# Kernel optimization log

Measured on AMD Instinct MI355X. Metric: run time of the kernel, lower is better.

## Reference

```python
import jax, jax.numpy as jnp
import numpy as np

SYLL_V, WORD_V, K = 10000, 20000, 10
SYLL_D, WORD_D, H = 64, 32, 64  # H = hidden_dim // 2 per direction
B, T = 256, 512
IN_D = SYLL_D + WORD_D


def lstm_dir(x, w_ih, w_hh, b_ih, b_hh, reverse):
    # x: [B,T,D]; w_ih: [4H,D]; w_hh: [4H,H]; PyTorch gate order i,f,g,o
    b, t, _ = x.shape
    h = w_hh.shape[1]
    xp = jnp.einsum('btd,gd->btg', x, w_ih) + b_ih + b_hh  # [B,T,4H]
    if reverse:
        xp = xp[:, ::-1]
    def step(carry, xt):
        hs, cs = carry
        g = xt + hs @ w_hh.T
        i, f, gg, o = jnp.split(g, 4, axis=-1)
        i = jax.nn.sigmoid(i); f = jax.nn.sigmoid(f)
        gg = jnp.tanh(gg); o = jax.nn.sigmoid(o)
        cs = f * cs + i * gg
        hs = o * jnp.tanh(cs)
        return (hs, cs), hs
    h0 = jnp.zeros((b, h), x.dtype)
    _, hseq = jax.lax.scan(step, (h0, h0), jnp.swapaxes(xp, 0, 1))
    hseq = jnp.swapaxes(hseq, 0, 1)  # [B,T,H]
    if reverse:
        hseq = hseq[:, ::-1]
    return hseq


def crf_llh(emissions, tags, mask, start_t, end_t, trans):
    # torchcrf log-likelihood, batch_first. emissions [B,T,K], tags [B,T], mask [B,T] bool
    b, t, k = emissions.shape
    mf = mask.astype(emissions.dtype)
    ar = jnp.arange(b)
    # numerator: score of the given tag path
    num = start_t[tags[:, 0]] + emissions[ar, 0, tags[:, 0]]
    e_tag = jnp.take_along_axis(emissions, tags[:, :, None], axis=2)[:, :, 0]  # [B,T]
    tr = trans[tags[:, :-1], tags[:, 1:]]  # [B,T-1]
    num = num + jnp.sum(mf[:, 1:] * (tr + e_tag[:, 1:]), axis=1)
    seq_len = jnp.sum(mask.astype(jnp.int32), axis=1)
    last_tags = jnp.take_along_axis(tags, (seq_len - 1)[:, None], axis=1)[:, 0]
    num = num + end_t[last_tags]
    # denominator: log partition via forward algorithm (sequential logsumexp scan)
    alpha0 = start_t[None, :] + emissions[:, 0]  # [B,K]
    def step(alpha, inp):
        em_t, m_t = inp  # [B,K], [B]
        nxt = jax.nn.logsumexp(alpha[:, :, None] + trans[None] + em_t[:, None, :], axis=1)
        return jnp.where(m_t[:, None], nxt, alpha), None
    alpha, _ = jax.lax.scan(
        step, alpha0,
        (jnp.swapaxes(emissions[:, 1:], 0, 1), jnp.swapaxes(mask[:, 1:], 0, 1)))
    den = jax.nn.logsumexp(alpha + end_t[None, :], axis=1)
    return num - den


def setup_inputs() -> dict:
    key = jax.random.key(0)
    ks = jax.random.split(key, 20)
    s = 0.1
    syll_emb = jax.random.normal(ks[0], (SYLL_V, SYLL_D), jnp.float32) * s
    syll_emb = syll_emb.at[0].set(0.0)  # padding_idx
    word_emb = jax.random.normal(ks[1], (WORD_V, WORD_D), jnp.float32) * s
    word_emb = word_emb.at[0].set(0.0)
    def lstm_params(i):
        return (jax.random.normal(ks[i], (4 * H, IN_D), jnp.float32) * s,
                jax.random.normal(ks[i + 1], (4 * H, H), jnp.float32) * s,
                jax.random.normal(ks[i + 2], (4 * H,), jnp.float32) * s,
                jax.random.normal(ks[i + 3], (4 * H,), jnp.float32) * s)
    w_ih_f, w_hh_f, b_ih_f, b_hh_f = lstm_params(2)
    w_ih_b, w_hh_b, b_ih_b, b_hh_b = lstm_params(6)
    W_tag = jax.random.normal(ks[10], (K, 2 * H), jnp.float32) * s
    b_tag = jax.random.normal(ks[11], (K,), jnp.float32) * s
    crf_start = jax.random.normal(ks[12], (K,), jnp.float32) * s
    crf_end = jax.random.normal(ks[13], (K,), jnp.float32) * s
    crf_trans = jax.random.normal(ks[14], (K, K), jnp.float32) * s
    return {
        'syll_input': jax.random.randint(ks[15], (B, T), 0, SYLL_V),
        'word_input': jax.random.randint(ks[16], (B, T), 0, WORD_V),
        'tags': jax.random.randint(ks[17], (B, T), 0, K),
        'mask': jnp.ones((B, T), jnp.bool_),
        'syll_emb': syll_emb, 'word_emb': word_emb,
        'w_ih_f': w_ih_f, 'w_hh_f': w_hh_f, 'b_ih_f': b_ih_f, 'b_hh_f': b_hh_f,
        'w_ih_b': w_ih_b, 'w_hh_b': w_hh_b, 'b_ih_b': b_ih_b, 'b_hh_b': b_hh_b,
        'W_tag': W_tag, 'b_tag': b_tag,
        'crf_start': crf_start, 'crf_end': crf_end, 'crf_trans': crf_trans,
    }


def reference(syll_input, word_input, tags, mask,
              syll_emb, word_emb,
              w_ih_f, w_hh_f, b_ih_f, b_hh_f,
              w_ih_b, w_hh_b, b_ih_b, b_hh_b,
              W_tag, b_tag, crf_start, crf_end, crf_trans):
    combined = jnp.concatenate([syll_emb[syll_input], word_emb[word_input]], axis=2)  # [B,T,96]
    h_f = lstm_dir(combined, w_ih_f, w_hh_f, b_ih_f, b_hh_f, reverse=False)
    h_b = lstm_dir(combined, w_ih_b, w_hh_b, b_ih_b, b_hh_b, reverse=True)
    lstm_out = jnp.concatenate([h_f, h_b], axis=2)  # [B,T,128]
    emissions = jnp.einsum('bth,kh->btk', lstm_out, W_tag) + b_tag
    llh = crf_llh(emissions, tags, mask, crf_start, crf_end, crf_trans)
    return -jnp.mean(llh)  # reduction='mean', negated
```

## Files before the change

kernel.cpp:

```cpp
#include <hip/hip_runtime.h>

typedef unsigned short ushort_t;
typedef unsigned int uint_t;
typedef __attribute__((ext_vector_type(8))) short short8;
typedef __attribute__((ext_vector_type(4))) float f32x4;
typedef __fp16 fp16x2 __attribute__((ext_vector_type(2)));
typedef __fp16 fp16x4 __attribute__((ext_vector_type(4)));

#define B_SZ 256
#define T_LEN 512
#define Hd 64
#define IND 96
#define G4 256
#define KT 10
#define SYLL_V 10000
#define WORD_V 20000
#define TP 520

#define L2E  1.4426950408889634f
#define L2E2 2.8853900817779268f

#define U16_PS_F 0
#define U16_PS_B (SYLL_V*G4)
#define U16_PW_F (2*SYLL_V*G4)
#define U16_PW_B (2*SYLL_V*G4 + WORD_V*G4)
#define U16_TAB_END (2*SYLL_V*G4 + 2*WORD_V*G4)
#define F_EM   (U16_TAB_END/2)
#define F_OMEGA (F_EM + B_SZ*T_LEN*KT)
#define F_S1   (F_OMEGA + B_SZ*64*100)
#define F_END  (F_S1 + B_SZ*64)
#define F_OFFS (F_END + (B_SZ*T_LEN*2*Hd)/2)
#define F_WBUF (F_OFFS + 2*B_SZ*TP*2)
#define F_BIAS (F_WBUF + 49152*4)

template <int V> struct ic { static constexpr int v = V; };

__device__ __forceinline__ ushort_t f2bf(float f) {
    uint_t u = __float_as_uint(f);
    uint_t r = (u + 0x7FFFu + ((u >> 16) & 1u)) >> 16;
    return (ushort_t)r;
}
__device__ __forceinline__ short8 cvt8(const float* p) {
    float4 x0 = *(const float4*)&p[0];
    float4 x1 = *(const float4*)&p[4];
    short8 f;
    f[0] = (short)f2bf(x0.x); f[1] = (short)f2bf(x0.y);
    f[2] = (short)f2bf(x0.z); f[3] = (short)f2bf(x0.w);
    f[4] = (short)f2bf(x1.x); f[5] = (short)f2bf(x1.y);
    f[6] = (short)f2bf(x1.z); f[7] = (short)f2bf(x1.w);
    return f;
}
__device__ __forceinline__ short8 cvt8s(const float* p, float sc) {
    float4 x0 = *(const float4*)&p[0];
    float4 x1 = *(const float4*)&p[4];
    short8 f;
    f[0] = (short)f2bf(x0.x*sc); f[1] = (short)f2bf(x0.y*sc);
    f[2] = (short)f2bf(x0.z*sc); f[3] = (short)f2bf(x0.w*sc);
    f[4] = (short)f2bf(x1.x*sc); f[5] = (short)f2bf(x1.y*sc);
    f[6] = (short)f2bf(x1.z*sc); f[7] = (short)f2bf(x1.w*sc);
    return f;
}

__global__ __launch_bounds__(256) void wprep_kernel(
    const float* __restrict__ w_ih_f, const float* __restrict__ w_ih_b,
    const float* __restrict__ b_ih_f, const float* __restrict__ b_hh_f,
    const float* __restrict__ b_ih_b, const float* __restrict__ b_hh_b,
    short8* __restrict__ wbuf, float* __restrict__ biasbuf)
{
    const int dir = blockIdx.x;
    const float* __restrict__ wih = dir ? w_ih_b : w_ih_f;
    const float* __restrict__ bi = dir ? b_ih_b : b_ih_f;
    const float* __restrict__ bh = dir ? b_hh_b : b_hh_f;
    const int tid = threadIdx.x;
    const int w = tid >> 6;
    const int l = tid & 63;
    const int rg = l >> 4;
    const int c = l & 15;

    {
        int s = tid;
        int g = 64 * (s & 3) + (s >> 2);
        float gsc = ((s & 3) == 2) ? L2E2 : -L2E;
        biasbuf[dir * 256 + s] = 0.5f * (bi[g] + bh[g]) * gsc;
    }
#pragma unroll
    for (int mt = 0; mt < 4; mt++) {
        int s = 64 * w + 16 * mt + c;
        int g = 64 * (s & 3) + (s >> 2);
        float gsc = ((s & 3) == 2) ? L2E2 : -L2E;
#pragma unroll
        for (int ch = 0; ch < 3; ch++) {
            const float* wp = &wih[g * 96 + ch * 32 + rg * 8];
            float4 x0 = *(const float4*)&wp[0];
            float4 x1 = *(const float4*)&wp[4];
            float vv[8] = {x0.x, x0.y, x0.z, x0.w, x1.x, x1.y, x1.z, x1.w};
            short8 h8, l8;
#pragma unroll
            for (int j = 0; j < 8; j++) {
                float sv = vv[j] * gsc;
                ushort_t hb2 = f2bf(sv);
                h8[j] = (short)hb2;
                l8[j] = (short)f2bf(sv - __uint_as_float((uint_t)hb2 << 16));
            }
            int base = (((dir * 4 + w) * 4 + mt) * 3 + ch) * 2;
            wbuf[(size_t)(base + 0) * 64 + l] = h8;
            wbuf[(size_t)(base + 1) * 64 + l] = l8;
        }
    }
}

__global__ __launch_bounds__(128) void offs_kernel(
    const int* __restrict__ syll, const int* __restrict__ word,
    int2* __restrict__ offs)
{
    const int bid = blockIdx.x;
    const int dir = bid & 1;
    const int b = bid >> 1;
    int2* __restrict__ o = offs + (size_t)(dir * B_SZ + b) * TP;
    for (int t = threadIdx.x; t < TP; t += 128) {
        int tc = t > T_LEN - 1 ? T_LEN - 1 : t;
        int p = dir ? (T_LEN - 1 - tc) : tc;
        int2 v;
        v.x = syll[b * T_LEN + p] << 9;
        v.y = word[b * T_LEN + p] << 9;
        o[t] = v;
    }
}

template <int D, int CH0, int NCH>
__global__ __launch_bounds__(256) void proj_mfma(
    const float* __restrict__ emb,
    const short8* __restrict__ wbuf, const float* __restrict__ biasbuf,
    ushort_t* __restrict__ out_f, ushort_t* __restrict__ out_b)
{
    const int dir = blockIdx.y;
    ushort_t* __restrict__ out = dir ? out_b : out_f;
    const int v0 = blockIdx.x * 16;
    const int tid = threadIdx.x;
    const int w = tid >> 6;
    const int l = tid & 63;
    const int rg = l >> 4;
    const int c = l & 15;

    __shared__ __align__(16) ushort_t Xh[16][D + 8];
    for (int i = tid; i < 16 * D; i += 256) {
        int row = i / D, k = i - row * D;
        Xh[row][k] = f2bf(emb[(size_t)v0 * D + i]);
    }

    short8 Ah[4][NCH], Al[4][NCH];
    f32x4 bias[4];
#pragma unroll
    for (int mt = 0; mt < 4; mt++) {
#pragma unroll
        for (int ch = 0; ch < NCH; ch++) {
            int base = (((dir * 4 + w) * 4 + mt) * 3 + (CH0 + ch)) * 2;
            Ah[mt][ch] = wbuf[(size_t)(base + 0) * 64 + l];
            Al[mt][ch] = wbuf[(size_t)(base + 1) * 64 + l];
        }
        bias[mt] = *(const f32x4*)&biasbuf[dir * 256 + 64 * w + 16 * mt + 4 * rg];
    }
    __syncthreads();

#pragma unroll
    for (int mt = 0; mt < 4; mt++) {
        f32x4 acc = bias[mt];
#pragma unroll
        for (int ch = 0; ch < NCH; ch++) {
            short8 Bf = *(const short8*)&Xh[c][ch * 32 + rg * 8];
            acc = __builtin_amdgcn_mfma_f32_16x16x32_bf16(Ah[mt][ch], Bf, acc, 0, 0, 0);
            acc = __builtin_amdgcn_mfma_f32_16x16x32_bf16(Al[mt][ch], Bf, acc, 0, 0, 0);
        }
        fp16x2 p0 = __builtin_amdgcn_cvt_pkrtz(acc[0], acc[1]);
        fp16x2 p1 = __builtin_amdgcn_cvt_pkrtz(acc[2], acc[3]);
        uint2 o;
        o.x = *(uint_t*)&p0;
        o.y = *(uint_t*)&p1;
        *(uint2*)&out[(size_t)(v0 + c) * G4 + 64 * w + 16 * mt + 4 * rg] = o;
    }
}

__global__ __launch_bounds__(256, 1) void lstm_kernel(
    const float* __restrict__ w_hh_f, const float* __restrict__ w_hh_b,
    const ushort_t* __restrict__ tab_u16, const int2* __restrict__ offs,
    ushort_t* __restrict__ h_out)
{
    const int dir = blockIdx.x & 1;
    const int bA = (blockIdx.x >> 1) * 4;
    const int tid = threadIdx.x;
    const int w = tid >> 6;
    const int l = tid & 63;
    const int rg = l >> 4;
    const int c = l & 15;
    const int cell = 16 * w + c;
    const int celloff = cell * 8;

    const char* __restrict__ tsb = (const char*)(tab_u16 + (dir ? U16_PS_B : U16_PS_F));
    const char* __restrict__ twb = (const char*)(tab_u16 + (dir ? U16_PW_B : U16_PW_F));
    const float* __restrict__ whh = dir ? w_hh_b : w_hh_f;

    short8 bfrag[4][2];
#pragma unroll
    for (int tau = 0; tau < 4; tau++) {
        const float sc = (tau == 2) ? L2E2 : -L2E;
#pragma unroll
        for (int chk = 0; chk < 2; chk++)
            bfrag[tau][chk] = cvt8s(whh + (size_t)(64 * tau + cell) * Hd + chk * 32 + rg * 8, sc);
    }

    __shared__ __align__(16) ushort_t h_lds[2][16][72];
    for (int i = tid; i < 2 * 16 * 72; i += 256) ((ushort_t*)h_lds)[i] = 0;

    const int chain = bA + rg;
    const int p0 = dir ? (T_LEN - 1) : 0;
    const int2* __restrict__ op = offs + (size_t)(dir * B_SZ + chain) * TP;

    fp16x4 tS[4], tW[4];
    int2 ix[4];
#pragma unroll
    for (int j = 0; j < 4; j++) {
        int2 o = op[j];
        tS[j] = *(const fp16x4*)(tsb + ((size_t)o.x + celloff));
        tW[j] = *(const fp16x4*)(twb + ((size_t)o.y + celloff));
        ix[j] = op[j + 4];
    }

    float cst = 0.f;
    ushort_t* hp = h_out + ((size_t)(chain * T_LEN + p0) * 2 + dir) * Hd + cell;
    const int hstep = dir ? -128 : 128;
    const f32x4 zro = {0.f, 0.f, 0.f, 0.f};
    __syncthreads();

    auto step = [&](auto STC, int t) {
        constexpr int ST = decltype(STC)::v;
        fp16x4 pp = tS[ST] + tW[ST];
        float ps0 = (float)pp[0];
        float ps1 = (float)pp[1];
        float ps2 = (float)pp[2];
        float ps3 = (float)pp[3];
        tS[ST] = *(const fp16x4*)(tsb + ((size_t)ix[ST].x + celloff));
        tW[ST] = *(const fp16x4*)(twb + ((size_t)ix[ST].y + celloff));
        ix[ST] = op[t + 8];

        f32x4 cc0 = {ps0, 0.f, 0.f, 0.f};
        f32x4 cc1 = {ps1, 0.f, 0.f, 0.f};
        f32x4 cc2 = {ps2, 0.f, 0.f, 0.f};
        f32x4 cc3 = {ps3, 0.f, 0.f, 0.f};
        const ushort_t* hrow = &h_lds[t & 1][c][0];
        short8 a0 = *(const short8*)(hrow + rg * 8);
        short8 a1 = *(const short8*)(hrow + 32 + rg * 8);
        f32x4 p00 = __builtin_amdgcn_mfma_f32_16x16x32_bf16(a0, bfrag[0][0], cc0, 0, 0, 0);
        f32x4 p10 = __builtin_amdgcn_mfma_f32_16x16x32_bf16(a0, bfrag[1][0], cc1, 0, 0, 0);
        f32x4 p20 = __builtin_amdgcn_mfma_f32_16x16x32_bf16(a0, bfrag[2][0], cc2, 0, 0, 0);
        f32x4 p30 = __builtin_amdgcn_mfma_f32_16x16x32_bf16(a0, bfrag[3][0], cc3, 0, 0, 0);
        f32x4 p01 = __builtin_amdgcn_mfma_f32_16x16x32_bf16(a1, bfrag[0][1], zro, 0, 0, 0);
        f32x4 p11 = __builtin_amdgcn_mfma_f32_16x16x32_bf16(a1, bfrag[1][1], zro, 0, 0, 0);
        f32x4 p21 = __builtin_amdgcn_mfma_f32_16x16x32_bf16(a1, bfrag[2][1], zro, 0, 0, 0);
        f32x4 p31 = __builtin_amdgcn_mfma_f32_16x16x32_bf16(a1, bfrag[3][1], zro, 0, 0, 0);

        float ai = p00[0] + p01[0];
        float af = p10[0] + p11[0];
        float ag = fminf(p20[0] + p21[0], 60.0f);
        float ao = p30[0] + p31[0];
        float ei = __builtin_amdgcn_exp2f(ai);
        float ef = __builtin_amdgcn_exp2f(af);
        float Eg = __builtin_amdgcn_exp2f(ag);
        float eo = __builtin_amdgcn_exp2f(ao);
        float e3 = 1.0f + ef;
        float pe = (1.0f + ei) * (1.0f + Eg);
        float num = __builtin_fmaf(Eg - 1.0f, e3, cst * pe);
        float cn = num * __builtin_amdgcn_rcpf(e3 * pe);
        cst = cn;
        float t2 = fminf(cn * L2E2, 60.0f);
        float E2 = __builtin_amdgcn_exp2f(t2);
        float h = (E2 - 1.0f) * __builtin_amdgcn_rcpf((1.0f + eo) * (1.0f + E2));

        ushort_t hb = f2bf(h);
        h_lds[(t + 1) & 1][4 * rg][cell] = hb;
        *hp = hb;
        hp += hstep;
        __builtin_amdgcn_sched_barrier(0);
        asm volatile("s_waitcnt lgkmcnt(0)" ::: "memory");
        __builtin_amdgcn_s_barrier();
        __builtin_amdgcn_sched_barrier(0);
    };

    for (int t = 0; t < T_LEN; t += 4) {
        step(ic<0>{}, t);
        step(ic<1>{}, t + 1);
        step(ic<2>{}, t + 2);
        step(ic<3>{}, t + 3);
    }
}

#define EMIS_G 4
__global__ __launch_bounds__(64) void emis_kernel(
    const ushort_t* __restrict__ hseq, const float* __restrict__ W_tag,
    const float* __restrict__ b_tag, float* __restrict__ em)
{
    const int l = threadIdx.x;
    const int rg = l >> 4;
    const int n = l & 15;

    short8 bf[4];
#pragma unroll
    for (int ch = 0; ch < 4; ch++) {
        if (n < KT) bf[ch] = cvt8(W_tag + (size_t)n * 128 + ch * 32 + rg * 8);
        else { short8 z = {0,0,0,0,0,0,0,0}; bf[ch] = z; }
    }
    const float btv = (n < KT) ? b_tag[n] : 0.f;

#pragma unroll
    for (int gi = 0; gi < EMIS_G; gi++) {
        const int row0 = (blockIdx.x * EMIS_G + gi) * 16;
        const ushort_t* __restrict__ ar = hseq + (size_t)(row0 + n) * 128 + rg * 8;
        short8 a0 = *(const short8*)&ar[0];
        short8 a1 = *(const short8*)&ar[32];
        short8 a2 = *(const short8*)&ar[64];
        short8 a3 = *(const short8*)&ar[96];
        f32x4 acc = {btv, btv, btv, btv};
        acc = __builtin_amdgcn_mfma_f32_16x16x32_bf16(a0, bf[0], acc, 0, 0, 0);
        acc = __builtin_amdgcn_mfma_f32_16x16x32_bf16(a1, bf[1], acc, 0, 0, 0);
        acc = __builtin_amdgcn_mfma_f32_16x16x32_bf16(a2, bf[2], acc, 0, 0, 0);
        acc = __builtin_amdgcn_mfma_f32_16x16x32_bf16(a3, bf[3], acc, 0, 0, 0);
        if (n < KT) {
#pragma unroll
            for (int r = 0; r < 4; r++)
                em[(size_t)(row0 + 4 * rg + r) * KT + n] = acc[r];
        }
    }
}

__global__ __launch_bounds__(64) void crf_stage1(
    const float* __restrict__ em, const float* __restrict__ trans,
    float* __restrict__ Omega, float* __restrict__ S1)
{
    __shared__ float etT[KT * 12];
    const int tid = threadIdx.x;
    for (int i = tid; i < KT * 12; i += 64) etT[i] = 0.f;
    __syncthreads();
    for (int i = tid; i < 100; i += 64) {
        int jj = i / 10, k = i % 10;
        etT[k * 12 + jj] = __expf(trans[i]);
    }
    __syncthreads();

    const int id = blockIdx.x * 64 + tid;
    const int b = id >> 6, c = id & 63;
    const int t0 = (c == 0) ? 1 : c * 8;
    const int nt = (c == 0) ? 7 : 8;

    float run[10][10];
    float s = 0.f;

    float ecur[10];
    {
        const float* r = em + (size_t)(b * T_LEN + t0) * KT;
#pragma unroll
        for (int k = 0; k < 10; k++) ecur[k] = r[k];
    }
    {
        float mx = ecur[0];
#pragma unroll
        for (int k = 1; k < 10; k++) mx = fmaxf(mx, ecur[k]);
        s += mx;
        float ee[10];
#pragma unroll
        for (int k = 0; k < 10; k++) ee[k] = __expf(ecur[k] - mx);
#pragma unroll
        for (int jj = 0; jj < 10; jj++)
#pragma unroll
            for (int k = 0; k < 10; k++) run[jj][k] = etT[k * 12 + jj] * ee[k];
    }
    float enx[10];
    if (nt > 1) {
        const float* r = em + (size_t)(b * T_LEN + t0 + 1) * KT;
#pragma unroll
        for (int k = 0; k < 10; k++) enx[k] = r[k];
    }
    for (int li = 1; li < nt; li++) {
        float mx = enx[0];
#pragma unroll
        for (int k = 1; k < 10; k++) mx = fmaxf(mx, enx[k]);
        s += mx;
        float ee[10];
#pragma unroll
        for (int k = 0; k < 10; k++) ee[k] = __expf(enx[k] - mx);
        if (li + 1 < nt) {
            const float* r = em + (size_t)(b * T_LEN + t0 + li + 1) * KT;
#pragma unroll
            for (int k = 0; k < 10; k++) enx[k] = r[k];
        }
#pragma unroll
        for (int i = 0; i < 10; i++) {
            float outp[10];
#pragma unroll
            for (int k = 0; k < 10; k++) {
                float sum = 0.f;
#pragma unroll
                for (int jj = 0; jj < 10; jj++) sum += run[i][jj] * etT[k * 12 + jj];
                outp[k] = sum * ee[k];
            }
#pragma unroll
            for (int k = 0; k < 10; k++) run[i][k] = outp[k];
        }
    }
    float m = run[0][0];
#pragma unroll
    for (int i = 0; i < 10; i++)
#pragma unroll
        for (int k = 0; k < 10; k++) m = fmaxf(m, run[i][k]);
    float inv = 1.0f / m;
    s += __logf(m);
#pragma unroll
    for (int i = 0; i < 10; i++)
#pragma unroll
        for (int k = 0; k < 10; k++) Omega[(size_t)id * 100 + i * 10 + k] = run[i][k] * inv;
    S1[id] = s;
}

__global__ __launch_bounds__(256) void crf_stage2(
    const float* __restrict__ Omega, const float* __restrict__ S1,
    const float* __restrict__ em, const int* __restrict__ tags,
    const float* __restrict__ start_t, const float* __restrict__ end_t,
    const float* __restrict__ trans, float* __restrict__ out)
{
    const int b = blockIdx.x;
    const int tid = threadIdx.x;
    __shared__ float bufA[64 * 120];
    __shared__ float bufB[32 * 120];
    __shared__ float sh_red[4];
    __shared__ float sh_s;
    __shared__ float scl_sh[32];
    __shared__ float lg_sh[32];
    __shared__ float lg_acc_sh;

    for (int idx = tid; idx < 6400; idx += 256) {
        int c = idx / 100, e = idx % 100;
        bufA[c * 120 + (e / 10) * 12 + (e % 10)] = Omega[(size_t)(b * 64 + c) * 100 + e];
    }
    if (tid < 64) {
        float v = S1[b * 64 + tid];
        for (int off = 32; off; off >>= 1) v += __shfl_down(v, off);
        if (tid == 0) sh_s = v;
    }
    if (tid == 0) lg_acc_sh = 0.f;
    __syncthreads();

    float* src = bufA;
    float* dst = bufB;
    for (int n = 32; n >= 1; n >>= 1) {
        for (int idx = tid; idx < n * 100; idx += 256) {
            int p = idx / 100, e = idx % 100, i = e / 10, k = e % 10;
            const float* A = src + (2 * p) * 120;
            const float* Bm = src + (2 * p + 1) * 120;
            float sum = 0.f;
#pragma unroll
            for (int jj = 0; jj < 10; jj++) sum += A[i * 12 + jj] * Bm[jj * 12 + k];
            dst[p * 120 + i * 12 + k] = sum;
        }
        __syncthreads();
        if (n == 32 || n == 8 || n == 2) {
            if (tid < n) {
                const float* M = dst + tid * 120;
                float mx = 0.f;
                for (int i = 0; i < 10; i++)
                    for (int k = 0; k < 10; k++) mx = fmaxf(mx, M[i * 12 + k]);
                scl_sh[tid] = 1.0f / mx;
                lg_sh[tid] = __logf(mx);
            }
            __syncthreads();
            if (tid == 0) {
                float s = 0.f;
                for (int p = 0; p < n; p++) s += lg_sh[p];
                lg_acc_sh += s;
            }
            for (int idx = tid; idx < n * 100; idx += 256) {
                int p = idx / 100, e = idx % 100;
                dst[p * 120 + (e / 10) * 12 + (e % 10)] *= scl_sh[p];
            }
            __syncthreads();
        }
        float* t_ = src; src = dst; dst = t_;
    }

    float den = 0.f;
    if (tid < 64) {
        float val = 0.f;
        float mx0 = 0.f;
        if (tid < 10) {
            mx0 = -1e30f;
            for (int jj = 0; jj < 10; jj++) mx0 = fmaxf(mx0, start_t[jj] + em[(size_t)(b * T_LEN) * KT + jj]);
            for (int jj = 0; jj < 10; jj++) {
                float v0 = __expf(start_t[jj] + em[(size_t)(b * T_LEN) * KT + jj] - mx0);
                val += v0 * src[jj * 12 + tid];
            }
            val *= __expf(end_t[tid]);
        }
        for (int off = 8; off; off >>= 1) val += __shfl_down(val, off);
        if (tid == 0) den = __logf(val) + mx0 + sh_s + lg_acc_sh;
    }

    float part = 0.f;
    const int* __restrict__ tg = tags + b * T_LEN;
    for (int t = tid; t < T_LEN; t += 256) {
        int cur = tg[t];
        if (t == 0) part += start_t[cur] + em[(size_t)(b * T_LEN) * KT + cur];
        else part += trans[tg[t - 1] * KT + cur] + em[(size_t)(b * T_LEN + t) * KT + cur];
        if (t == T_LEN - 1) part += end_t[cur];
    }
    for (int off = 32; off; off >>= 1) part += __shfl_down(part, off);
    if ((tid & 63) == 0) sh_red[tid >> 6] = part;
    __syncthreads();
    if (tid == 0) {
        float num = sh_red[0] + sh_red[1] + sh_red[2] + sh_red[3];
        float llh = num - den;
        atomicAdd(out, llh * (-1.0f / 256.0f));
    }
}

extern "C" void kernel_launch(void* const* d_in, const int* in_sizes, int n_in,
                              void* d_out, int out_size, void* d_ws, size_t ws_size,
                              hipStream_t stream) {
    const int* syll      = (const int*)d_in[0];
    const int* word      = (const int*)d_in[1];
    const int* tags      = (const int*)d_in[2];
    const float* syll_emb = (const float*)d_in[4];
    const float* word_emb = (const float*)d_in[5];
    const float* w_ih_f  = (const float*)d_in[6];
    const float* w_hh_f  = (const float*)d_in[7];
    const float* b_ih_f  = (const float*)d_in[8];
    const float* b_hh_f  = (const float*)d_in[9];
    const float* w_ih_b  = (const float*)d_in[10];
    const float* w_hh_b  = (const float*)d_in[11];
    const float* b_ih_b  = (const float*)d_in[12];
    const float* b_hh_b  = (const float*)d_in[13];
    const float* W_tag   = (const float*)d_in[14];
    const float* b_tag   = (const float*)d_in[15];
    const float* crf_start = (const float*)d_in[16];
    const float* crf_end   = (const float*)d_in[17];
    const float* crf_trans = (const float*)d_in[18];

    float* out = (float*)d_out;
    float* ws = (float*)d_ws;
    ushort_t* tab = (ushort_t*)ws;
    ushort_t* hseq = (ushort_t*)(ws + F_END);
    int2* offs = (int2*)(ws + F_OFFS);
    short8* wbuf = (short8*)(ws + F_WBUF);
    float* biasbuf = ws + F_BIAS;

    hipMemsetAsync(d_out, 0, sizeof(float), stream);

    wprep_kernel<<<2, 256, 0, stream>>>(
        w_ih_f, w_ih_b, b_ih_f, b_hh_f, b_ih_b, b_hh_b, wbuf, biasbuf);

    offs_kernel<<<B_SZ * 2, 128, 0, stream>>>(syll, word, offs);

    proj_mfma<64, 0, 2><<<dim3(SYLL_V / 16, 2), 256, 0, stream>>>(
        syll_emb, wbuf, biasbuf, tab + U16_PS_F, tab + U16_PS_B);
    proj_mfma<32, 2, 1><<<dim3(WORD_V / 16, 2), 256, 0, stream>>>(
        word_emb, wbuf, biasbuf, tab + U16_PW_F, tab + U16_PW_B);

    lstm_kernel<<<B_SZ * 2 / 4, 256, 0, stream>>>(
        w_hh_f, w_hh_b, tab, offs, hseq);

    emis_kernel<<<B_SZ * T_LEN / (16 * EMIS_G), 64, 0, stream>>>(
        hseq, W_tag, b_tag, ws + F_EM);

    crf_stage1<<<256, 64, 0, stream>>>(ws + F_EM, crf_trans, ws + F_OMEGA, ws + F_S1);

    crf_stage2<<<B_SZ, 256, 0, stream>>>(
        ws + F_OMEGA, ws + F_S1, ws + F_EM, tags, crf_start, crf_end, crf_trans, out);
}
```

Baseline: 304.0 us.

## Fuse emission projection and both CRF stages into one kernel using LDS

Replaces the emission kernel and the two CRF stage kernels with a single kernel in which each block handles two batch rows. Emissions are computed with MFMA into shared memory, the chunked transfer-matrix products run in registers, and the tree reduction reuses the same LDS buffer. This removes two kernel launches and the global round trips for emissions, Omega and S1. In exchange the grid drops to 128 blocks of 256 threads with large LDS use, so fewer waves are in flight, and only half the threads do the stage-1 work.

Measured after the change: 312.3 us. 1.03x slower.

```diff
diff --git a/kernel.cpp b/kernel.cpp
--- a/kernel.cpp
+++ b/kernel.cpp
@@ -25,10 +25,7 @@
 #define U16_PW_F (2*SYLL_V*G4)
 #define U16_PW_B (2*SYLL_V*G4 + WORD_V*G4)
 #define U16_TAB_END (2*SYLL_V*G4 + 2*WORD_V*G4)
-#define F_EM   (U16_TAB_END/2)
-#define F_OMEGA (F_EM + B_SZ*T_LEN*KT)
-#define F_S1   (F_OMEGA + B_SZ*64*100)
-#define F_END  (F_S1 + B_SZ*64)
+#define F_END  (U16_TAB_END/2)
 #define F_OFFS (F_END + (B_SZ*T_LEN*2*Hd)/2)
 #define F_WBUF (F_OFFS + 2*B_SZ*TP*2)
 #define F_BIAS (F_WBUF + 49152*4)
@@ -293,14 +290,34 @@
     }
 }
 
-#define EMIS_G 4
-__global__ __launch_bounds__(64) void emis_kernel(
+__global__ __launch_bounds__(256) void crf_fused(
     const ushort_t* __restrict__ hseq, const float* __restrict__ W_tag,
-    const float* __restrict__ b_tag, float* __restrict__ em)
+    const float* __restrict__ b_tag, const float* __restrict__ trans,
+    const int* __restrict__ tags, const float* __restrict__ start_t,
+    const float* __restrict__ end_t, float* __restrict__ out)
 {
-    const int l = threadIdx.x;
+    const int tid = threadIdx.x;
+    const int w = tid >> 6;
+    const int l = tid & 63;
     const int rg = l >> 4;
     const int n = l & 15;
+
+    __shared__ __align__(16) float em_l[1024 * 12];
+    __shared__ float etT[120];
+    __shared__ float e0_sh[2][10];
+    __shared__ float scl_sh[32];
+    __shared__ float lg_sh[32];
+    __shared__ float sh_s[2];
+    __shared__ float num_sh[2][2];
+    __shared__ float lg_acc;
+    __shared__ float den_sh[2];
+
+    for (int i = tid; i < 120; i += 256) etT[i] = 0.f;
+    __syncthreads();
+    for (int i = tid; i < 100; i += 256) {
+        int jj = i / 10, k = i % 10;
+        etT[k * 12 + jj] = __expf(trans[i]);
+    }
 
     short8 bf[4];
 #pragma unroll
@@ -309,11 +326,11 @@
         else { short8 z = {0,0,0,0,0,0,0,0}; bf[ch] = z; }
     }
     const float btv = (n < KT) ? b_tag[n] : 0.f;
-
-#pragma unroll
-    for (int gi = 0; gi < EMIS_G; gi++) {
-        const int row0 = (blockIdx.x * EMIS_G + gi) * 16;
-        const ushort_t* __restrict__ ar = hseq + (size_t)(row0 + n) * 128 + rg * 8;
+    const size_t gbase = (size_t)blockIdx.x * 1024;
+#pragma unroll 4
+    for (int gi = 0; gi < 16; gi++) {
+        const int row0 = w * 256 + gi * 16;
+        const ushort_t* __restrict__ ar = hseq + (gbase + row0 + n) * 128 + rg * 8;
         short8 a0 = *(const short8*)&ar[0];
         short8 a1 = *(const short8*)&ar[32];
         short8 a2 = *(const short8*)&ar[64];
@@ -326,197 +343,171 @@
         if (n < KT) {
 #pragma unroll
             for (int r = 0; r < 4; r++)
-                em[(size_t)(row0 + 4 * rg + r) * KT + n] = acc[r];
-        }
-    }
-}
-
-__global__ __launch_bounds__(64) void crf_stage1(
-    const float* __restrict__ em, const float* __restrict__ trans,
-    float* __restrict__ Omega, float* __restrict__ S1)
-{
-    __shared__ float etT[KT * 12];
-    const int tid = threadIdx.x;
-    for (int i = tid; i < KT * 12; i += 64) etT[i] = 0.f;
+                em_l[(row0 + 4 * rg + r) * 12 + n] = acc[r];
+        }
+    }
     __syncthreads();
-    for (int i = tid; i < 100; i += 64) {
-        int jj = i / 10, k = i % 10;
-        etT[k * 12 + jj] = __expf(trans[i]);
-    }
-    __syncthreads();
-
-    const int id = blockIdx.x * 64 + tid;
-    const int b = id >> 6, c = id & 63;
-    const int t0 = (c == 0) ? 1 : c * 8;
-    const int nt = (c == 0) ? 7 : 8;
-
+
+    const int bl = tid >> 6;
+    const int c = tid & 63;
+    const bool active = tid < 128;
     float run[10][10];
     float s = 0.f;
-
-    float ecur[10];
+    if (active) {
+        const int t0 = (c == 0) ? 1 : c * 8;
+        const int nt = (c == 0) ? 7 : 8;
+        const float* __restrict__ eb = &em_l[(bl * 512) * 12];
+        float ecur[10];
+#pragma unroll
+        for (int k = 0; k < 10; k++) ecur[k] = eb[t0 * 12 + k];
+        {
+            float mx = ecur[0];
+#pragma unroll
+            for (int k = 1; k < 10; k++) mx = fmaxf(mx, ecur[k]);
+            s += mx;
+            float ee[10];
+#pragma unroll
+            for (int k = 0; k < 10; k++) ee[k] = __expf(ecur[k] - mx);
+#pragma unroll
+            for (int jj = 0; jj < 10; jj++)
+#pragma unroll
+                for (int k = 0; k < 10; k++) run[jj][k] = etT[k * 12 + jj] * ee[k];
+        }
+        for (int li = 1; li < nt; li++) {
+            float enx[10];
+#pragma unroll
+            for (int k = 0; k < 10; k++) enx[k] = eb[(t0 + li) * 12 + k];
+            float mx = enx[0];
+#pragma unroll
+            for (int k = 1; k < 10; k++) mx = fmaxf(mx, enx[k]);
+            s += mx;
+            float ee[10];
+#pragma unroll
+            for (int k = 0; k < 10; k++) ee[k] = __expf(enx[k] - mx);
+#pragma unroll
+            for (int i = 0; i < 10; i++) {
+                float outp[10];
+#pragma unroll
+                for (int k = 0; k < 10; k++) {
+                    float sum = 0.f;
+#pragma unroll
+                    for (int jj = 0; jj < 10; jj++) sum += run[i][jj] * etT[k * 12 + jj];
+                    outp[k] = sum * ee[k];
+                }
+#pragma unroll
+                for (int k = 0; k < 10; k++) run[i][k] = outp[k];
+            }
+        }
+        float m = run[0][0];
+#pragma unroll
+        for (int i = 0; i < 10; i++)
+#pragma unroll
+            for (int k = 0; k < 10; k++) m = fmaxf(m, run[i][k]);
+        float inv = 1.0f / m;
+        s += __logf(m);
+#pragma unroll
+        for (int i = 0; i < 10; i++)
+#pragma unroll
+            for (int k = 0; k < 10; k++) run[i][k] *= inv;
+    }
+
     {
-        const float* r = em + (size_t)(b * T_LEN + t0) * KT;
-#pragma unroll
-        for (int k = 0; k < 10; k++) ecur[k] = r[k];
-    }
-    {
-        float mx = ecur[0];
-#pragma unroll
-        for (int k = 1; k < 10; k++) mx = fmaxf(mx, ecur[k]);
-        s += mx;
-        float ee[10];
-#pragma unroll
-        for (int k = 0; k < 10; k++) ee[k] = __expf(ecur[k] - mx);
-#pragma unroll
-        for (int jj = 0; jj < 10; jj++)
-#pragma unroll
-            for (int k = 0; k < 10; k++) run[jj][k] = etT[k * 12 + jj] * ee[k];
-    }
-    float enx[10];
-    if (nt > 1) {
-        const float* r = em + (size_t)(b * T_LEN + t0 + 1) * KT;
-#pragma unroll
-        for (int k = 0; k < 10; k++) enx[k] = r[k];
-    }
-    for (int li = 1; li < nt; li++) {
-        float mx = enx[0];
-#pragma unroll
-        for (int k = 1; k < 10; k++) mx = fmaxf(mx, enx[k]);
-        s += mx;
-        float ee[10];
-#pragma unroll
-        for (int k = 0; k < 10; k++) ee[k] = __expf(enx[k] - mx);
-        if (li + 1 < nt) {
-            const float* r = em + (size_t)(b * T_LEN + t0 + li + 1) * KT;
-#pragma unroll
-            for (int k = 0; k < 10; k++) enx[k] = r[k];
-        }
-#pragma unroll
-        for (int i = 0; i < 10; i++) {
-            float outp[10];
-#pragma unroll
-            for (int k = 0; k < 10; k++) {
+        const int blc = w >> 1;
+        const int b2 = blockIdx.x * 2 + blc;
+        const float* __restrict__ eb = &em_l[(blc * 512) * 12];
+        const int* __restrict__ tg = tags + b2 * T_LEN;
+        float part = 0.f;
+        for (int t = l + (w & 1) * 64; t < T_LEN; t += 128) {
+            int cur = tg[t];
+            float ev = eb[t * 12 + cur];
+            if (t == 0) part += start_t[cur] + ev;
+            else part += trans[tg[t - 1] * KT + cur] + ev;
+            if (t == T_LEN - 1) part += end_t[cur];
+        }
+        for (int off = 32; off; off >>= 1) part += __shfl_down(part, off);
+        if (l == 0) num_sh[blc][w & 1] = part;
+    }
+    if (tid < 20) {
+        int blc = tid / 10, jj = tid % 10;
+        e0_sh[blc][jj] = em_l[(blc * 512) * 12 + jj];
+    }
+    if (active) {
+        float v = s;
+        for (int off = 32; off; off >>= 1) v += __shfl_down(v, off);
+        if (c == 0) sh_s[bl] = v;
+    }
+
+    float* bufA = em_l;
+    float* bufB = em_l + 7680;
+    float llh_acc = 0.f;
+    for (int blc = 0; blc < 2; blc++) {
+        __syncthreads();
+        if (active && bl == blc) {
+#pragma unroll
+            for (int i = 0; i < 10; i++)
+#pragma unroll
+                for (int k = 0; k < 10; k++) bufA[c * 120 + i * 12 + k] = run[i][k];
+        }
+        if (tid == 0) lg_acc = 0.f;
+        __syncthreads();
+
+        float* src = bufA;
+        float* dst = bufB;
+        for (int nn = 32; nn >= 1; nn >>= 1) {
+            for (int idx = tid; idx < nn * 100; idx += 256) {
+                int p = idx / 100, e = idx % 100, i = e / 10, k = e % 10;
+                const float* A = src + (2 * p) * 120;
+                const float* Bm = src + (2 * p + 1) * 120;
                 float sum = 0.f;
 #pragma unroll
-                for (int jj = 0; jj < 10; jj++) sum += run[i][jj] * etT[k * 12 + jj];
-                outp[k] = sum * ee[k];
-            }
-#pragma unroll
-            for (int k = 0; k < 10; k++) run[i][k] = outp[k];
-        }
-    }
-    float m = run[0][0];
-#pragma unroll
-    for (int i = 0; i < 10; i++)
-#pragma unroll
-        for (int k = 0; k < 10; k++) m = fmaxf(m, run[i][k]);
-    float inv = 1.0f / m;
-    s += __logf(m);
-#pragma unroll
-    for (int i = 0; i < 10; i++)
-#pragma unroll
-        for (int k = 0; k < 10; k++) Omega[(size_t)id * 100 + i * 10 + k] = run[i][k] * inv;
-    S1[id] = s;
-}
-
-__global__ __launch_bounds__(256) void crf_stage2(
-    const float* __restrict__ Omega, const float* __restrict__ S1,
-    const float* __restrict__ em, const int* __restrict__ tags,
-    const float* __restrict__ start_t, const float* __restrict__ end_t,
-    const float* __restrict__ trans, float* __restrict__ out)
-{
-    const int b = blockIdx.x;
-    const int tid = threadIdx.x;
-    __shared__ float bufA[64 * 120];
-    __shared__ float bufB[32 * 120];
-    __shared__ float sh_red[4];
-    __shared__ float sh_s;
-    __shared__ float scl_sh[32];
-    __shared__ float lg_sh[32];
-    __shared__ float lg_acc_sh;
-
-    for (int idx = tid; idx < 6400; idx += 256) {
-        int c = idx / 100, e = idx % 100;
-        bufA[c * 120 + (e / 10) * 12 + (e % 10)] = Omega[(size_t)(b * 64 + c) * 100 + e];
-    }
-    if (tid < 64) {
-        float v = S1[b * 64 + tid];
-        for (int off = 32; off; off >>= 1) v += __shfl_down(v, off);
-        if (tid == 0) sh_s = v;
-    }
-    if (tid == 0) lg_acc_sh = 0.f;
-    __syncthreads();
-
-    float* src = bufA;
-    float* dst = bufB;
-    for (int n = 32; n >= 1; n >>= 1) {
-        for (int idx = tid; idx < n * 100; idx += 256) {
-            int p = idx / 100, e = idx % 100, i = e / 10, k = e % 10;
-            const float* A = src + (2 * p) * 120;
-            const float* Bm = src + (2 * p + 1) * 120;
-            float sum = 0.f;
-#pragma unroll
-            for (int jj = 0; jj < 10; jj++) sum += A[i * 12 + jj] * Bm[jj * 12 + k];
-            dst[p * 120 + i * 12 + k] = sum;
-        }
-        __syncthreads();
-        if (n == 32 || n == 8 || n == 2) {
-            if (tid < n) {
-                const float* M = dst + tid * 120;
-                float mx = 0.f;
-                for (int i = 0; i < 10; i++)
-                    for (int k = 0; k < 10; k++) mx = fmaxf(mx, M[i * 12 + k]);
-                scl_sh[tid] = 1.0f / mx;
-                lg_sh[tid] = __logf(mx);
+                for (int jj = 0; jj < 10; jj++) sum += A[i * 12 + jj] * Bm[jj * 12 + k];
+                dst[p * 120 + i * 12 + k] = sum;
             }
             __syncthreads();
-            if (tid == 0) {
-                float s = 0.f;
-                for (int p = 0; p < n; p++) s += lg_sh[p];
-                lg_acc_sh += s;
+            if (nn == 32 || nn == 8 || nn == 2) {
+                if (tid < nn) {
+                    const float* M = dst + tid * 120;
+                    float mx = 0.f;
+                    for (int i = 0; i < 10; i++)
+                        for (int k = 0; k < 10; k++) mx = fmaxf(mx, M[i * 12 + k]);
+                    scl_sh[tid] = 1.0f / mx;
+                    lg_sh[tid] = __logf(mx);
+                }
+                __syncthreads();
+                if (tid == 0) {
+                    float ssum = 0.f;
+                    for (int p = 0; p < nn; p++) ssum += lg_sh[p];
+                    lg_acc += ssum;
+                }
+                for (int idx = tid; idx < nn * 100; idx += 256) {
+                    int p = idx / 100, e = idx % 100;
+                    dst[p * 120 + (e / 10) * 12 + (e % 10)] *= scl_sh[p];
+                }
+                __syncthreads();
             }
-            for (int idx = tid; idx < n * 100; idx += 256) {
-                int p = idx / 100, e = idx % 100;
-                dst[p * 120 + (e / 10) * 12 + (e % 10)] *= scl_sh[p];
+            float* t_ = src; src = dst; dst = t_;
+        }
+
+        if (tid < 64) {
+            float val = 0.f;
+            float mx0 = 0.f;
+            if (tid < 10) {
+                mx0 = -1e30f;
+                for (int jj = 0; jj < 10; jj++) mx0 = fmaxf(mx0, start_t[jj] + e0_sh[blc][jj]);
+                for (int jj = 0; jj < 10; jj++) {
+                    float v0 = __expf(start_t[jj] + e0_sh[blc][jj] - mx0);
+                    val += v0 * src[jj * 12 + tid];
+                }
+                val *= __expf(end_t[tid]);
             }
-            __syncthreads();
-        }
-        float* t_ = src; src = dst; dst = t_;
-    }
-
-    float den = 0.f;
-    if (tid < 64) {
-        float val = 0.f;
-        float mx0 = 0.f;
-        if (tid < 10) {
-            mx0 = -1e30f;
-            for (int jj = 0; jj < 10; jj++) mx0 = fmaxf(mx0, start_t[jj] + em[(size_t)(b * T_LEN) * KT + jj]);
-            for (int jj = 0; jj < 10; jj++) {
-                float v0 = __expf(start_t[jj] + em[(size_t)(b * T_LEN) * KT + jj] - mx0);
-                val += v0 * src[jj * 12 + tid];
-            }
-            val *= __expf(end_t[tid]);
-        }
-        for (int off = 8; off; off >>= 1) val += __shfl_down(val, off);
-        if (tid == 0) den = __logf(val) + mx0 + sh_s + lg_acc_sh;
-    }
-
-    float part = 0.f;
-    const int* __restrict__ tg = tags + b * T_LEN;
-    for (int t = tid; t < T_LEN; t += 256) {
-        int cur = tg[t];
-        if (t == 0) part += start_t[cur] + em[(size_t)(b * T_LEN) * KT + cur];
-        else part += trans[tg[t - 1] * KT + cur] + em[(size_t)(b * T_LEN + t) * KT + cur];
-        if (t == T_LEN - 1) part += end_t[cur];
-    }
-    for (int off = 32; off; off >>= 1) part += __shfl_down(part, off);
-    if ((tid & 63) == 0) sh_red[tid >> 6] = part;
-    __syncthreads();
-    if (tid == 0) {
-        float num = sh_red[0] + sh_red[1] + sh_red[2] + sh_red[3];
-        float llh = num - den;
-        atomicAdd(out, llh * (-1.0f / 256.0f));
-    }
+            for (int off = 8; off; off >>= 1) val += __shfl_down(val, off);
+            if (tid == 0) den_sh[blc] = __logf(val) + mx0 + sh_s[blc] + lg_acc;
+        }
+        __syncthreads();
+        if (tid == 0)
+            llh_acc += (num_sh[blc][0] + num_sh[blc][1]) - den_sh[blc];
+    }
+    if (tid == 0) atomicAdd(out, llh_acc * (-1.0f / 256.0f));
 }
 
 extern "C" void kernel_launch(void* const* d_in, const int* in_sizes, int n_in,
@@ -564,11 +555,6 @@
     lstm_kernel<<<B_SZ * 2 / 4, 256, 0, stream>>>(
         w_hh_f, w_hh_b, tab, offs, hseq);
 
-    emis_kernel<<<B_SZ * T_LEN / (16 * EMIS_G), 64, 0, stream>>>(
-        hseq, W_tag, b_tag, ws + F_EM);
-
-    crf_stage1<<<256, 64, 0, stream>>>(ws + F_EM, crf_trans, ws + F_OMEGA, ws + F_S1);
-
-    crf_stage2<<<B_SZ, 256, 0, stream>>>(
-        ws + F_OMEGA, ws + F_S1, ws + F_EM, tags, crf_start, crf_end, crf_trans, out);
-}
+    crf_fused<<<B_SZ / 2, 256, 0, stream>>>(
+        hseq, W_tag, b_tag, crf_trans, tags, crf_start, crf_end, out);
+}
```
